# Kernel tuning notes

Hardware: AMD Instinct MI355X
Metric: run time of the kernel (lower is better)

## Reference

```python
import jax, jax.numpy as jnp
import numpy as np

K = 1024      # num_embeddings
D = 256       # embedding_dim
B, T = 64, 2048
DECAY = 0.99
EPS = 1e-5
COMMIT = 0.25


def setup_inputs() -> dict:
    key = jax.random.key(0)
    k1, k2, k3 = jax.random.split(key, 3)
    inputs = jax.random.normal(k1, (D, B, T), dtype=jnp.float32)
    embedding = jax.random.normal(k2, (K, D), dtype=jnp.float32)        # nn.Embedding weight (normal_())
    ema_w = jax.random.normal(k3, (K, D), dtype=jnp.float32)            # _ema_w (normal_())
    ema_cluster_size = jnp.zeros((K,), dtype=jnp.float32)               # _ema_cluster_size buffer
    return {"inputs": inputs, "embedding": embedding,
            "ema_cluster_size": ema_cluster_size, "ema_w": ema_w}


def reference(inputs, embedding, ema_cluster_size, ema_w):
    # inputs: [D, B, T] -> permute(1,2,0) -> [B, T, D]
    x = jnp.transpose(inputs, (1, 2, 0))
    flat = x.reshape(-1, D)                                  # [N, D], N = B*T

    # squared-euclidean distances to codebook: [N, K]
    distances = (jnp.sum(flat * flat, axis=1, keepdims=True)
                 + jnp.sum(embedding * embedding, axis=1)
                 - 2.0 * (flat @ embedding.T))

    encoding_indices = jnp.argmin(distances, axis=1)         # [N]
    encodings = jax.nn.one_hot(encoding_indices, K, dtype=jnp.float32)  # [N, K]

    # --- EMA codebook update (training path; detached in torch via nn.Parameter rewrap) ---
    counts = jnp.sum(encodings, axis=0)                      # [K]
    new_cs = ema_cluster_size * DECAY + (1.0 - DECAY) * counts
    n = jnp.sum(new_cs)
    new_cs = (new_cs + EPS) / (n + K * EPS) * n              # Laplace smoothing
    dw = encodings.T @ flat                                  # [K, D] scatter-add of assigned vectors
    new_ema_w = ema_w * DECAY + (1.0 - DECAY) * dw
    new_embedding = new_ema_w / new_cs[:, None]              # updated codebook

    # quantize with the UPDATED codebook (as in the torch training path)
    quantized = (encodings @ new_embedding).reshape(x.shape)  # [B, T, D]

    e_latent_loss = jnp.mean((jax.lax.stop_gradient(quantized) - x) ** 2)
    vq_loss = COMMIT * e_latent_loss

    # straight-through estimator
    quantized_st = x + jax.lax.stop_gradient(quantized - x)

    avg_probs = jnp.mean(encodings, axis=0)                  # [K]
    perplexity = jnp.exp(-jnp.sum(avg_probs * jnp.log(avg_probs + 1e-10)))

    quantized_out = jnp.transpose(quantized_st, (2, 0, 1))   # back to [D, B, T]
    return (vq_loss, quantized_out, perplexity, encodings, distances,
            encoding_indices, new_cs, new_ema_w, new_embedding)
```

## Files before the change

kernel.cpp:

```cpp
#include <hip/hip_runtime.h>
#include <hip/hip_bf16.h>
#include <cstdint>
#include <cstddef>

#define N_ROWS 131072
#define K_CB   1024
#define D_DIM  256
#define ND_TOT 33554432ull
#define NK_TOT 134217728ull
#define CHUNK  64

typedef __attribute__((ext_vector_type(8))) short short8;
typedef __attribute__((ext_vector_type(16))) float f32x16;
typedef __attribute__((address_space(3))) uint32_t lds_u32_t;
typedef const __attribute__((address_space(1))) uint32_t glb_u32_t;

static __device__ __forceinline__ float omd() { return (float)(1.0 - 0.99); }

static __device__ __forceinline__ float bf2f(ushort u) {
  union { uint32_t i; float f; } x; x.i = ((uint32_t)u) << 16; return x.f;
}
static __device__ __forceinline__ ushort f2bf(float f) {
  uint32_t x = __builtin_bit_cast(uint32_t, f);
  return (ushort)((x + 0x7fffu + ((x >> 16) & 1u)) >> 16);
}
static __device__ __forceinline__ void split3(float v, ushort& h, ushort& m, ushort& l) {
  h = f2bf(v);
  float r1 = v - bf2f(h);
  m = f2bf(r1);
  l = f2bf(r1 - bf2f(m));
}

__global__ __launch_bounds__(256) void esq_k(const float* __restrict__ emb, float* __restrict__ esq) {
  int k = blockIdx.x * 4 + (threadIdx.x >> 6);
  int lane = threadIdx.x & 63;
  const float* er = emb + (size_t)k * D_DIM;
  float s = 0.f;
#pragma unroll
  for (int t = 0; t < 4; ++t) { float v = er[t * 64 + lane]; s += v * v; }
  for (int off = 32; off; off >>= 1) s += __shfl_down(s, off);
  if (lane == 0) esq[k] = s;
}

__global__ __launch_bounds__(256) void split_a_k(const float* __restrict__ in,
    ushort* __restrict__ aH, ushort* __restrict__ aM, ushort* __restrict__ aL,
    float* __restrict__ xsq) {
  __shared__ float tile[128][65];
  __shared__ float part[4][64];
  int n0 = blockIdx.x * 64, d0 = blockIdx.y * 128;
  int lane = threadIdx.x & 63, grp = threadIdx.x >> 6;
  float ps = 0.f;
#pragma unroll
  for (int r = 0; r < 32; ++r) {
    int d = grp * 32 + r;
    float v = in[(size_t)(d0 + d) * N_ROWS + n0 + lane];
    tile[d][lane] = v;
    ps += v * v;
  }
  part[grp][lane] = ps;
  __syncthreads();
  if (grp == 0) {
    float s = part[0][lane] + part[1][lane] + part[2][lane] + part[3][lane];
    atomicAdd(&xsq[n0 + lane], s);
  }
#pragma unroll
  for (int r = 0; r < 16; ++r) {
    int nr = grp * 16 + r;
    float v0 = tile[lane * 2][nr], v1 = tile[lane * 2 + 1][nr];
    ushort h0, m0, l0, h1, m1, l1;
    split3(v0, h0, m0, l0);
    split3(v1, h1, m1, l1);
    size_t o = (size_t)(n0 + nr) * D_DIM + d0 + lane * 2;
    *(uint32_t*)&aH[o] = (uint32_t)h0 | ((uint32_t)h1 << 16);
    *(uint32_t*)&aM[o] = (uint32_t)m0 | ((uint32_t)m1 << 16);
    *(uint32_t*)&aL[o] = (uint32_t)l0 | ((uint32_t)l1 << 16);
  }
}

__global__ __launch_bounds__(256) void split_b_k(const float* __restrict__ emb,
    ushort* __restrict__ bH, ushort* __restrict__ bM) {
  int i = blockIdx.x * 256 + threadIdx.x;
  ushort h, m, l;
  split3(emb[i], h, m, l);
  bH[i] = h; bM[i] = m;
}

__global__ __launch_bounds__(256, 2) void mfma_dist_k(
    const ushort* __restrict__ aH, const ushort* __restrict__ aM,
    const ushort* __restrict__ bH, const ushort* __restrict__ bM,
    const float* __restrict__ xsq, const float* __restrict__ esq,
    float* __restrict__ dist, float* __restrict__ pminv, int* __restrict__ pmink) {
  __shared__ __align__(16) char lds[65536];
  const int tid = threadIdx.x;
  const int wv = tid >> 6, l = tid & 63;
  const int l31 = l & 31, hb = l >> 5;
  const int wr = wv >> 1, wc = wv & 1;

  int t0 = (blockIdx.x & 7) * 1024 + (blockIdx.x >> 3);
  const int bx = t0 >> 3, by = t0 & 7;
  const int n0 = bx * 128, k0 = by * 128;

  int gOff[4], lOff[4];
#pragma unroll
  for (int i = 0; i < 4; ++i) {
    int ch = i * 256 + tid;
    int r = ch >> 3, s = ch & 7;
    gOff[i] = r * 512 + ((s ^ (r & 7)) << 4);
    lOff[i] = (i * 256 + (tid & 192)) << 4;
  }

  const char* pa0 = (const char*)aH + (size_t)n0 * 512;
  const char* pa1 = (const char*)aM + (size_t)n0 * 512;
  const char* pb0 = (const char*)bH + (size_t)k0 * 512;
  const char* pb1 = (const char*)bM + (size_t)k0 * 512;

  f32x16 acc[2][2];
#pragma unroll
  for (int a = 0; a < 2; ++a)
#pragma unroll
    for (int b = 0; b < 2; ++b)
#pragma unroll
      for (int e = 0; e < 16; ++e) acc[a][b][e] = 0.f;

  for (int kc = 0; kc < 4; ++kc) {
    const int kb = kc << 7;
    __syncthreads();
#pragma unroll
    for (int i = 0; i < 4; ++i) {
      __builtin_amdgcn_global_load_lds((glb_u32_t*)(pa0 + kb + gOff[i]), (lds_u32_t*)(lds + lOff[i]), 16, 0, 0);
      __builtin_amdgcn_global_load_lds((glb_u32_t*)(pa1 + kb + gOff[i]), (lds_u32_t*)(lds + 16384 + lOff[i]), 16, 0, 0);
      __builtin_amdgcn_global_load_lds((glb_u32_t*)(pb0 + kb + gOff[i]), (lds_u32_t*)(lds + 32768 + lOff[i]), 16, 0, 0);
      __builtin_amdgcn_global_load_lds((glb_u32_t*)(pb1 + kb + gOff[i]), (lds_u32_t*)(lds + 49152 + lOff[i]), 16, 0, 0);
    }
    __syncthreads();
#pragma unroll
    for (int ks = 0; ks < 4; ++ks) {
      short8 af[2][2], bf[2][2];
#pragma unroll
      for (int ar = 0; ar < 2; ++ar) {
        int row = wr * 64 + ar * 32 + l31;
        int byte = (((row << 7) + (ks << 5) + (hb << 4)) ^ ((row & 7) << 4));
        af[0][ar] = *(const short8*)(lds + byte);
        af[1][ar] = *(const short8*)(lds + 16384 + byte);
      }
#pragma unroll
      for (int bc = 0; bc < 2; ++bc) {
        int row = wc * 64 + bc * 32 + l31;
        int byte = (((row << 7) + (ks << 5) + (hb << 4)) ^ ((row & 7) << 4));
        bf[0][bc] = *(const short8*)(lds + 32768 + byte);
        bf[1][bc] = *(const short8*)(lds + 49152 + byte);
      }
#pragma unroll
      for (int ar = 0; ar < 2; ++ar)
#pragma unroll
        for (int bc = 0; bc < 2; ++bc) {
          acc[ar][bc] = __builtin_amdgcn_mfma_f32_32x32x16_bf16(af[0][ar], bf[0][bc], acc[ar][bc], 0, 0, 0);
          acc[ar][bc] = __builtin_amdgcn_mfma_f32_32x32x16_bf16(af[0][ar], bf[1][bc], acc[ar][bc], 0, 0, 0);
          acc[ar][bc] = __builtin_amdgcn_mfma_f32_32x32x16_bf16(af[1][ar], bf[0][bc], acc[ar][bc], 0, 0, 0);
          acc[ar][bc] = __builtin_amdgcn_mfma_f32_32x32x16_bf16(af[1][ar], bf[1][bc], acc[ar][bc], 0, 0, 0);
        }
    }
  }

  float es[2];
#pragma unroll
  for (int bc = 0; bc < 2; ++bc) es[bc] = esq[k0 + wc * 64 + bc * 32 + l31];

#pragma unroll
  for (int ar = 0; ar < 2; ++ar) {
    float minv[16];
    int mink[16];
#pragma unroll
    for (int r = 0; r < 16; ++r) { minv[r] = INFINITY; mink[r] = 0x7fffffff; }
#pragma unroll
    for (int r = 0; r < 16; ++r) {
      int rowo = (r & 3) + ((r >> 2) << 3) + (hb << 2);
      int grow = n0 + wr * 64 + ar * 32 + rowo;
      float xs = xsq[grow];
#pragma unroll
      for (int bc = 0; bc < 2; ++bc) {
        int gcol = k0 + wc * 64 + bc * 32 + l31;
        float dv = xs + es[bc] - 2.f * acc[ar][bc][r];
        dist[(size_t)grow * K_CB + gcol] = dv;
        if (dv < minv[r]) { minv[r] = dv; mink[r] = gcol; }
      }
    }
#pragma unroll
    for (int off = 1; off < 32; off <<= 1) {
#pragma unroll
      for (int r = 0; r < 16; ++r) {
        float ov = __shfl_xor(minv[r], off);
        int ok = __shfl_xor(mink[r], off);
        if (ov < minv[r] || (ov == minv[r] && ok < mink[r])) { minv[r] = ov; mink[r] = ok; }
      }
    }
    if (l31 == 0) {
      int slot = by * 2 + wc;
#pragma unroll
      for (int r = 0; r < 16; ++r) {
        int grow = n0 + wr * 64 + ar * 32 + (r & 3) + ((r >> 2) << 3) + (hb << 2);
        pminv[(size_t)slot * N_ROWS + grow] = minv[r];
        pmink[(size_t)slot * N_ROWS + grow] = mink[r];
      }
    }
  }
}

__global__ __launch_bounds__(256) void argmin_fin_k(const float* __restrict__ pminv,
                                                    const int* __restrict__ pmink,
                                                    int* __restrict__ idx, float* __restrict__ idxf) {
  int n = blockIdx.x * 256 + threadIdx.x;
  float mv = INFINITY;
  int mi = 0x7fffffff;
#pragma unroll
  for (int s = 0; s < 16; ++s) {
    float v = pminv[(size_t)s * N_ROWS + n];
    int k = pmink[(size_t)s * N_ROWS + n];
    if (v < mv || (v == mv && k < mi)) { mv = v; mi = k; }
  }
  idx[n] = mi;
  idxf[n] = (float)mi;
}

__global__ __launch_bounds__(256) void scat_k(const int* __restrict__ idx, float* __restrict__ enc) {
  int n = blockIdx.x * 256 + threadIdx.x;
  enc[(size_t)n * K_CB + idx[n]] = 1.0f;
}

__global__ __launch_bounds__(256) void counts_k(const int* __restrict__ idx, unsigned* __restrict__ counts) {
  __shared__ unsigned h[K_CB];
  for (int i = threadIdx.x; i < K_CB; i += 256) h[i] = 0;
  __syncthreads();
  for (size_t i = (size_t)blockIdx.x * 256 + threadIdx.x; i < N_ROWS; i += (size_t)gridDim.x * 256)
    atomicAdd(&h[idx[i]], 1u);
  __syncthreads();
  for (int i = threadIdx.x; i < K_CB; i += 256) {
    unsigned v = h[i];
    if (v) atomicAdd(&counts[i], v);
  }
}

__global__ __launch_bounds__(1024) void prefix_k(const unsigned* __restrict__ counts,
                                                 int* __restrict__ start, int* __restrict__ cursor) {
  __shared__ int s[K_CB];
  int t = threadIdx.x;
  int v = (int)counts[t];
  s[t] = v;
  __syncthreads();
  for (int off = 1; off < K_CB; off <<= 1) {
    int x = (t >= off) ? s[t - off] : 0;
    __syncthreads();
    s[t] += x;
    __syncthreads();
  }
  int excl = s[t] - v;
  start[t] = excl;
  cursor[t] = excl;
  if (t == K_CB - 1) start[K_CB] = s[t];
}

__global__ __launch_bounds__(256) void scatter_k(const int* __restrict__ idx,
                                                 int* __restrict__ cursor, int* __restrict__ sorted) {
  int n = blockIdx.x * 256 + threadIdx.x;
  int pos = atomicAdd(&cursor[idx[n]], 1);
  sorted[pos] = n;
}

__global__ __launch_bounds__(256) void dwc_k(const ushort* __restrict__ aH,
                                             const ushort* __restrict__ aM,
                                             const ushort* __restrict__ aL,
                                             const int* __restrict__ sorted,
                                             const int* __restrict__ idx,
                                             float* __restrict__ dw) {
  __shared__ int s_n[CHUNK];
  __shared__ int s_k[CHUNK];
  int t = threadIdx.x;
  int r0 = blockIdx.x * CHUNK;
  if (t < CHUNK) {
    int n = sorted[r0 + t];
    s_n[t] = n;
    s_k[t] = idx[n];
  }
  __syncthreads();
  float acc = 0.f;
  for (int rb = 0; rb < CHUNK; rb += 8) {
    float v[8];
#pragma unroll
    for (int i = 0; i < 8; ++i) {
      size_t o = (size_t)s_n[rb + i] * D_DIM + t;
      v[i] = bf2f(aH[o]) + bf2f(aM[o]) + bf2f(aL[o]);
    }
#pragma unroll
    for (int i = 0; i < 8; ++i) {
      int r = rb + i;
      acc += v[i];
      if (r == CHUNK - 1 || s_k[r + 1] != s_k[r]) {
        atomicAdd(&dw[(size_t)s_k[r] * D_DIM + t], acc);
        acc = 0.f;
      }
    }
  }
}

__global__ __launch_bounds__(1024) void newcs_k(const float* __restrict__ ema_cs,
                                                const unsigned* __restrict__ counts,
                                                float* __restrict__ out_ncs,
                                                float* __restrict__ out_perp) {
  __shared__ float s[1024];
  int k = threadIdx.x;
  float c = (float)counts[k];
  float raw = 0.99f * ema_cs[k] + omd() * c;
  s[k] = raw;
  __syncthreads();
  for (int off = 512; off; off >>= 1) { if (k < off) s[k] += s[k + off]; __syncthreads(); }
  float nsum = s[0];
  __syncthreads();
  out_ncs[k] = (raw + 1e-5f) / (nsum + (float)(1024 * 1e-5)) * nsum;
  float p = c * (1.0f / 131072.0f);
  float t = p * logf(p + 1e-10f);
  s[k] = t;
  __syncthreads();
  for (int off = 512; off; off >>= 1) { if (k < off) s[k] += s[k + off]; __syncthreads(); }
  if (k == 0) out_perp[0] = expf(-s[0]);
}

__global__ __launch_bounds__(256) void newemb_k(const float* __restrict__ ema_w,
                                                const float* __restrict__ dw,
                                                const float* __restrict__ ncs,
                                                float* __restrict__ out_nw,
                                                float* __restrict__ out_ne) {
  int i = blockIdx.x * 256 + threadIdx.x;
  int k = i >> 8;
  float nw = 0.99f * ema_w[i] + omd() * dw[i];
  out_nw[i] = nw;
  out_ne[i] = nw / ncs[k];
}

__global__ __launch_bounds__(256) void quant_k(const float* __restrict__ in,
                                               const int* __restrict__ idx,
                                               const float* __restrict__ ne,
                                               float* __restrict__ qout,
                                               float* __restrict__ lossacc) {
  float lacc = 0.f;
  size_t stride = (size_t)gridDim.x * 256;
  for (size_t g = (size_t)blockIdx.x * 256 + threadIdx.x; g < (ND_TOT >> 2); g += stride) {
    size_t i = g << 2;
    int d = (int)(i >> 17);
    int n = (int)(i & (N_ROWS - 1));
    float4 x = *(const float4*)&in[i];
    int4 k4 = *(const int4*)&idx[n];
    float4 q;
    q.x = ne[(size_t)k4.x * D_DIM + d];
    q.y = ne[(size_t)k4.y * D_DIM + d];
    q.z = ne[(size_t)k4.z * D_DIM + d];
    q.w = ne[(size_t)k4.w * D_DIM + d];
    float4 o;
    o.x = x.x + (q.x - x.x);
    o.y = x.y + (q.y - x.y);
    o.z = x.z + (q.z - x.z);
    o.w = x.w + (q.w - x.w);
    *(float4*)&qout[i] = o;
    float dx = q.x - x.x, dy = q.y - x.y, dz = q.z - x.z, dwv = q.w - x.w;
    lacc += dx * dx + dy * dy + dz * dz + dwv * dwv;
  }
  for (int off = 32; off; off >>= 1) lacc += __shfl_down(lacc, off);
  __shared__ float w4[4];
  if ((threadIdx.x & 63) == 0) w4[threadIdx.x >> 6] = lacc;
  __syncthreads();
  if (threadIdx.x == 0) atomicAdd(lossacc, w4[0] + w4[1] + w4[2] + w4[3]);
}

__global__ void fin_k(const float* __restrict__ lossacc, float* __restrict__ out_loss) {
  out_loss[0] = 0.25f * lossacc[0] * (1.0f / 33554432.0f);
}

extern "C" void kernel_launch(void* const* d_in, const int* in_sizes, int n_in,
                              void* d_out, int out_size, void* d_ws, size_t ws_size,
                              hipStream_t stream) {
  const float* in     = (const float*)d_in[0];
  const float* emb    = (const float*)d_in[1];
  const float* ema_cs = (const float*)d_in[2];
  const float* ema_w  = (const float*)d_in[3];

  float* out = (float*)d_out;
  float* out_loss = out;
  float* out_q    = out + 1;
  float* out_perp = out + 33554433;
  float* out_enc  = out + 33554434;
  float* out_dist = out + 167772162;
  float* out_idx  = out + 301989890;
  float* out_ncs  = out + 302120962;
  float* out_nw   = out + 302121986;
  float* out_ne   = out + 302384130;

  char* w = (char*)d_ws;
  unsigned* counts  = (unsigned*)(w);
  float*    lossacc = (float*)(w + 4096);
  int*      cursor  = (int*)(w + 8192);
  int*      start   = (int*)(w + 12288);
  float*    xsq     = (float*)(w + 20480);
  float*    esq     = (float*)(w + 544768);
  int*      idx     = (int*)(w + 548864);
  int*      sorted  = (int*)(w + 1073152);
  float*    dw      = (float*)(w + 1597440);

  ushort* aH = (ushort*)((char*)out_enc + 8);
  ushort* aM = aH + ND_TOT;
  ushort* aL = aM + ND_TOT;
  ushort* bH = aL + ND_TOT;
  ushort* bM = bH + (K_CB * D_DIM);
  float*  pminv = (float*)(bM + (K_CB * D_DIM));
  int*    pmink = (int*)(pminv + 16 * (size_t)N_ROWS);

  hipMemsetAsync(d_ws, 0, 544768, stream);
  hipMemsetAsync(dw, 0, K_CB * D_DIM * 4, stream);

  split_a_k<<<dim3(N_ROWS / 64, 2), 256, 0, stream>>>(in, aH, aM, aL, xsq);
  split_b_k<<<K_CB * D_DIM / 256, 256, 0, stream>>>(emb, bH, bM);
  esq_k<<<K_CB / 4, 256, 0, stream>>>(emb, esq);
  mfma_dist_k<<<(N_ROWS / 128) * (K_CB / 128), 256, 0, stream>>>(
      aH, aM, bH, bM, xsq, esq, out_dist, pminv, pmink);
  argmin_fin_k<<<N_ROWS / 256, 256, 0, stream>>>(pminv, pmink, idx, out_idx);
  counts_k<<<64, 256, 0, stream>>>(idx, counts);
  prefix_k<<<1, 1024, 0, stream>>>(counts, start, cursor);
  scatter_k<<<N_ROWS / 256, 256, 0, stream>>>(idx, cursor, sorted);
  dwc_k<<<N_ROWS / CHUNK, 256, 0, stream>>>(aH, aM, aL, sorted, idx, dw);
  hipMemsetAsync(out_enc, 0, NK_TOT * 4, stream);
  scat_k<<<N_ROWS / 256, 256, 0, stream>>>(idx, out_enc);
  newcs_k<<<1, 1024, 0, stream>>>(ema_cs, counts, out_ncs, out_perp);
  newemb_k<<<K_CB * D_DIM / 256, 256, 0, stream>>>(ema_w, dw, out_ncs, out_nw, out_ne);
  quant_k<<<2048, 256, 0, stream>>>(in, idx, out_ne, out_q, lossacc);
  fin_k<<<1, 1, 0, stream>>>(lossacc, out_loss);
}
```

Baseline: 1.084 ms.

## Retile distance GEMM to 256x256 double-buffered 16x16 MFMA; fuse one-hot fill

The distance GEMM now uses 512-thread blocks computing 256x256 output tiles with 16x16x32 bf16 MFMAs. It double-buffers 128 KB of dynamic LDS so the next k-slice (one hi/mid plane pair per step) loads while the current one computes, and argmin partials are written to 16 slots as before. The aim is more operand reuse per LDS load and overlap of global-to-LDS transfer with MFMA work, at the cost of a larger register footprint and only one block per CU. Separately, the memset plus scatter that built the one-hot encodings is replaced by a single kernel that writes each row with vector stores, so the 512 MB output is written once instead of being zeroed and then scattered into.

New measurement: 1.171 ms. 8.0% more time.

```diff
diff --git a/kernel.cpp b/kernel.cpp
--- a/kernel.cpp
+++ b/kernel.cpp
@@ -11,7 +11,7 @@
 #define CHUNK  64
 
 typedef __attribute__((ext_vector_type(8))) short short8;
-typedef __attribute__((ext_vector_type(16))) float f32x16;
+typedef __attribute__((ext_vector_type(4))) float f32x4;
 typedef __attribute__((address_space(3))) uint32_t lds_u32_t;
 typedef const __attribute__((address_space(1))) uint32_t glb_u32_t;
 
@@ -85,122 +85,133 @@
   bH[i] = h; bM[i] = m;
 }
 
-__global__ __launch_bounds__(256, 2) void mfma_dist_k(
+__global__ __launch_bounds__(512, 2) void mfma_dist_k(
     const ushort* __restrict__ aH, const ushort* __restrict__ aM,
     const ushort* __restrict__ bH, const ushort* __restrict__ bM,
     const float* __restrict__ xsq, const float* __restrict__ esq,
     float* __restrict__ dist, float* __restrict__ pminv, int* __restrict__ pmink) {
-  __shared__ __align__(16) char lds[65536];
+  extern __shared__ __align__(16) char lds[];
   const int tid = threadIdx.x;
-  const int wv = tid >> 6, l = tid & 63;
-  const int l31 = l & 31, hb = l >> 5;
-  const int wr = wv >> 1, wc = wv & 1;
-
-  int t0 = (blockIdx.x & 7) * 1024 + (blockIdx.x >> 3);
-  const int bx = t0 >> 3, by = t0 & 7;
-  const int n0 = bx * 128, k0 = by * 128;
+  const int wid = tid >> 6, l = tid & 63;
+  const int l15 = l & 15, l4 = l >> 4;
+  const int wm = wid >> 2, wn = wid & 3;
+
+  int t0 = ((int)blockIdx.x & 7) * 256 + ((int)blockIdx.x >> 3);
+  const int bx = t0 >> 2, by = t0 & 3;
+  const int n0 = bx * 256, k0c = by * 256;
 
   int gOff[4], lOff[4];
 #pragma unroll
   for (int i = 0; i < 4; ++i) {
-    int ch = i * 256 + tid;
+    int ch = i * 512 + tid;
     int r = ch >> 3, s = ch & 7;
-    gOff[i] = r * 512 + ((s ^ (r & 7)) << 4);
-    lOff[i] = (i * 256 + (tid & 192)) << 4;
-  }
-
-  const char* pa0 = (const char*)aH + (size_t)n0 * 512;
-  const char* pa1 = (const char*)aM + (size_t)n0 * 512;
-  const char* pb0 = (const char*)bH + (size_t)k0 * 512;
-  const char* pb1 = (const char*)bM + (size_t)k0 * 512;
-
-  f32x16 acc[2][2];
-#pragma unroll
-  for (int a = 0; a < 2; ++a)
-#pragma unroll
-    for (int b = 0; b < 2; ++b)
-#pragma unroll
-      for (int e = 0; e < 16; ++e) acc[a][b][e] = 0.f;
-
-  for (int kc = 0; kc < 4; ++kc) {
-    const int kb = kc << 7;
+    int ss = s ^ ((r & 4) >> 1);
+    gOff[i] = r * 512 + (ss << 4);
+    lOff[i] = ch << 4;
+  }
+
+  const char* aPl[2] = { (const char*)aH + (size_t)n0 * 512,
+                         (const char*)aM + (size_t)n0 * 512 };
+  const char* bPl[2] = { (const char*)bH + (size_t)k0c * 512,
+                         (const char*)bM + (size_t)k0c * 512 };
+
+  f32x4 acc[8][4];
+#pragma unroll
+  for (int mi = 0; mi < 8; ++mi)
+#pragma unroll
+    for (int ni = 0; ni < 4; ++ni)
+#pragma unroll
+      for (int e = 0; e < 4; ++e) acc[mi][ni][e] = 0.f;
+
+#define STAGE(buf, kt)                                                          \
+  {                                                                             \
+    const char* pa = aPl[(kt) >> 3] + (((kt) & 3) << 7);                        \
+    const char* pb = bPl[((kt) >> 2) & 1] + (((kt) & 3) << 7);                  \
+    char* lb = lds + (buf) * 65536;                                             \
+    _Pragma("unroll")                                                           \
+    for (int i = 0; i < 4; ++i)                                                 \
+      __builtin_amdgcn_global_load_lds((glb_u32_t*)(pa + gOff[i]),              \
+          (lds_u32_t*)(lb + lOff[i]), 16, 0, 0);                                \
+    _Pragma("unroll")                                                           \
+    for (int i = 0; i < 4; ++i)                                                 \
+      __builtin_amdgcn_global_load_lds((glb_u32_t*)(pb + gOff[i]),              \
+          (lds_u32_t*)(lb + 32768 + lOff[i]), 16, 0, 0);                        \
+  }
+
+#define COMPUTE(buf)                                                            \
+  {                                                                             \
+    const char* LA = lds + (buf) * 65536;                                       \
+    const char* LB = LA + 32768;                                                \
+    _Pragma("unroll")                                                           \
+    for (int ks = 0; ks < 2; ++ks) {                                            \
+      short8 bf[4];                                                             \
+      _Pragma("unroll")                                                         \
+      for (int ni = 0; ni < 4; ++ni) {                                          \
+        int row = wn * 64 + ni * 16 + l15;                                      \
+        int L = row * 128 + ks * 64 + l4 * 16;                                  \
+        bf[ni] = *(const short8*)(LB + (L ^ ((row & 4) << 3)));                 \
+      }                                                                         \
+      _Pragma("unroll")                                                         \
+      for (int mi = 0; mi < 8; ++mi) {                                          \
+        int row = wm * 128 + mi * 16 + l15;                                     \
+        int L = row * 128 + ks * 64 + l4 * 16;                                  \
+        short8 af = *(const short8*)(LA + (L ^ ((row & 4) << 3)));              \
+        _Pragma("unroll")                                                       \
+        for (int ni = 0; ni < 4; ++ni)                                          \
+          acc[mi][ni] = __builtin_amdgcn_mfma_f32_16x16x32_bf16(af, bf[ni],     \
+                                                                acc[mi][ni], 0, 0, 0); \
+      }                                                                         \
+    }                                                                           \
+  }
+
+  STAGE(0, 0);
+  __syncthreads();
+  for (int kt = 0; kt < 16; ++kt) {
+    if (kt < 15) STAGE((kt + 1) & 1, kt + 1);
+    COMPUTE(kt & 1);
     __syncthreads();
-#pragma unroll
-    for (int i = 0; i < 4; ++i) {
-      __builtin_amdgcn_global_load_lds((glb_u32_t*)(pa0 + kb + gOff[i]), (lds_u32_t*)(lds + lOff[i]), 16, 0, 0);
-      __builtin_amdgcn_global_load_lds((glb_u32_t*)(pa1 + kb + gOff[i]), (lds_u32_t*)(lds + 16384 + lOff[i]), 16, 0, 0);
-      __builtin_amdgcn_global_load_lds((glb_u32_t*)(pb0 + kb + gOff[i]), (lds_u32_t*)(lds + 32768 + lOff[i]), 16, 0, 0);
-      __builtin_amdgcn_global_load_lds((glb_u32_t*)(pb1 + kb + gOff[i]), (lds_u32_t*)(lds + 49152 + lOff[i]), 16, 0, 0);
-    }
-    __syncthreads();
-#pragma unroll
-    for (int ks = 0; ks < 4; ++ks) {
-      short8 af[2][2], bf[2][2];
-#pragma unroll
-      for (int ar = 0; ar < 2; ++ar) {
-        int row = wr * 64 + ar * 32 + l31;
-        int byte = (((row << 7) + (ks << 5) + (hb << 4)) ^ ((row & 7) << 4));
-        af[0][ar] = *(const short8*)(lds + byte);
-        af[1][ar] = *(const short8*)(lds + 16384 + byte);
-      }
-#pragma unroll
-      for (int bc = 0; bc < 2; ++bc) {
-        int row = wc * 64 + bc * 32 + l31;
-        int byte = (((row << 7) + (ks << 5) + (hb << 4)) ^ ((row & 7) << 4));
-        bf[0][bc] = *(const short8*)(lds + 32768 + byte);
-        bf[1][bc] = *(const short8*)(lds + 49152 + byte);
-      }
-#pragma unroll
-      for (int ar = 0; ar < 2; ++ar)
-#pragma unroll
-        for (int bc = 0; bc < 2; ++bc) {
-          acc[ar][bc] = __builtin_amdgcn_mfma_f32_32x32x16_bf16(af[0][ar], bf[0][bc], acc[ar][bc], 0, 0, 0);
-          acc[ar][bc] = __builtin_amdgcn_mfma_f32_32x32x16_bf16(af[0][ar], bf[1][bc], acc[ar][bc], 0, 0, 0);
-          acc[ar][bc] = __builtin_amdgcn_mfma_f32_32x32x16_bf16(af[1][ar], bf[0][bc], acc[ar][bc], 0, 0, 0);
-          acc[ar][bc] = __builtin_amdgcn_mfma_f32_32x32x16_bf16(af[1][ar], bf[1][bc], acc[ar][bc], 0, 0, 0);
-        }
-    }
-  }
-
-  float es[2];
-#pragma unroll
-  for (int bc = 0; bc < 2; ++bc) es[bc] = esq[k0 + wc * 64 + bc * 32 + l31];
-
-#pragma unroll
-  for (int ar = 0; ar < 2; ++ar) {
-    float minv[16];
-    int mink[16];
-#pragma unroll
-    for (int r = 0; r < 16; ++r) { minv[r] = INFINITY; mink[r] = 0x7fffffff; }
-#pragma unroll
-    for (int r = 0; r < 16; ++r) {
-      int rowo = (r & 3) + ((r >> 2) << 3) + (hb << 2);
-      int grow = n0 + wr * 64 + ar * 32 + rowo;
+  }
+#undef STAGE
+#undef COMPUTE
+
+  float es[4];
+#pragma unroll
+  for (int ni = 0; ni < 4; ++ni) es[ni] = esq[k0c + wn * 64 + ni * 16 + l15];
+  const int slot = by * 4 + wn;
+
+#pragma unroll
+  for (int mi = 0; mi < 8; ++mi) {
+    float mv[4];
+    int mk[4];
+#pragma unroll
+    for (int reg = 0; reg < 4; ++reg) { mv[reg] = INFINITY; mk[reg] = 0x7fffffff; }
+#pragma unroll
+    for (int reg = 0; reg < 4; ++reg) {
+      int grow = n0 + wm * 128 + mi * 16 + l4 * 4 + reg;
       float xs = xsq[grow];
 #pragma unroll
-      for (int bc = 0; bc < 2; ++bc) {
-        int gcol = k0 + wc * 64 + bc * 32 + l31;
-        float dv = xs + es[bc] - 2.f * acc[ar][bc][r];
+      for (int ni = 0; ni < 4; ++ni) {
+        int gcol = k0c + wn * 64 + ni * 16 + l15;
+        float dv = xs + es[ni] - 2.f * acc[mi][ni][reg];
         dist[(size_t)grow * K_CB + gcol] = dv;
-        if (dv < minv[r]) { minv[r] = dv; mink[r] = gcol; }
+        if (dv < mv[reg]) { mv[reg] = dv; mk[reg] = gcol; }
       }
     }
 #pragma unroll
-    for (int off = 1; off < 32; off <<= 1) {
-#pragma unroll
-      for (int r = 0; r < 16; ++r) {
-        float ov = __shfl_xor(minv[r], off);
-        int ok = __shfl_xor(mink[r], off);
-        if (ov < minv[r] || (ov == minv[r] && ok < mink[r])) { minv[r] = ov; mink[r] = ok; }
+    for (int off = 1; off < 16; off <<= 1) {
+#pragma unroll
+      for (int reg = 0; reg < 4; ++reg) {
+        float ov = __shfl_xor(mv[reg], off);
+        int ok = __shfl_xor(mk[reg], off);
+        if (ov < mv[reg] || (ov == mv[reg] && ok < mk[reg])) { mv[reg] = ov; mk[reg] = ok; }
       }
     }
-    if (l31 == 0) {
-      int slot = by * 2 + wc;
-#pragma unroll
-      for (int r = 0; r < 16; ++r) {
-        int grow = n0 + wr * 64 + ar * 32 + (r & 3) + ((r >> 2) << 3) + (hb << 2);
-        pminv[(size_t)slot * N_ROWS + grow] = minv[r];
-        pmink[(size_t)slot * N_ROWS + grow] = mink[r];
+    if (l15 == 0) {
+#pragma unroll
+      for (int reg = 0; reg < 4; ++reg) {
+        int grow = n0 + wm * 128 + mi * 16 + l4 * 4 + reg;
+        pminv[(size_t)slot * N_ROWS + grow] = mv[reg];
+        pmink[(size_t)slot * N_ROWS + grow] = mk[reg];
       }
     }
   }
@@ -222,9 +233,16 @@
   idxf[n] = (float)mi;
 }
 
-__global__ __launch_bounds__(256) void scat_k(const int* __restrict__ idx, float* __restrict__ enc) {
-  int n = blockIdx.x * 256 + threadIdx.x;
-  enc[(size_t)n * K_CB + idx[n]] = 1.0f;
+__global__ __launch_bounds__(256) void enc_k(const int* __restrict__ idx, float* __restrict__ enc) {
+  int n = blockIdx.x * 2 + (threadIdx.x >> 7);
+  int c = (threadIdx.x & 127) * 8;
+  int k = idx[n];
+  float4 a = {0.f, 0.f, 0.f, 0.f}, b = {0.f, 0.f, 0.f, 0.f};
+  if (k >= c && k < c + 4) ((float*)&a)[k - c] = 1.0f;
+  else if (k >= c + 4 && k < c + 8) ((float*)&b)[k - c - 4] = 1.0f;
+  size_t o = (size_t)n * K_CB + c;
+  *(float4*)&enc[o] = a;
+  *(float4*)&enc[o + 4] = b;
 }
 
 __global__ __launch_bounds__(256) void counts_k(const int* __restrict__ idx, unsigned* __restrict__ counts) {
@@ -418,15 +436,14 @@
   split_a_k<<<dim3(N_ROWS / 64, 2), 256, 0, stream>>>(in, aH, aM, aL, xsq);
   split_b_k<<<K_CB * D_DIM / 256, 256, 0, stream>>>(emb, bH, bM);
   esq_k<<<K_CB / 4, 256, 0, stream>>>(emb, esq);
-  mfma_dist_k<<<(N_ROWS / 128) * (K_CB / 128), 256, 0, stream>>>(
+  mfma_dist_k<<<(N_ROWS / 256) * (K_CB / 256), 512, 131072, stream>>>(
       aH, aM, bH, bM, xsq, esq, out_dist, pminv, pmink);
   argmin_fin_k<<<N_ROWS / 256, 256, 0, stream>>>(pminv, pmink, idx, out_idx);
   counts_k<<<64, 256, 0, stream>>>(idx, counts);
   prefix_k<<<1, 1024, 0, stream>>>(counts, start, cursor);
   scatter_k<<<N_ROWS / 256, 256, 0, stream>>>(idx, cursor, sorted);
   dwc_k<<<N_ROWS / CHUNK, 256, 0, stream>>>(aH, aM, aL, sorted, idx, dw);
-  hipMemsetAsync(out_enc, 0, NK_TOT * 4, stream);
-  scat_k<<<N_ROWS / 256, 256, 0, stream>>>(idx, out_enc);
+  enc_k<<<N_ROWS / 2, 256, 0, stream>>>(idx, out_enc);
   newcs_k<<<1, 1024, 0, stream>>>(ema_cs, counts, out_ncs, out_perp);
   newemb_k<<<K_CB * D_DIM / 256, 256, 0, stream>>>(ema_w, dw, out_ncs, out_nw, out_ne);
   quant_k<<<2048, 256, 0, stream>>>(in, idx, out_ne, out_q, lossacc);
```
